# Kernel tuning notes

Hardware: AMD Instinct MI355X
Metric: run time of the kernel (lower is better)

The kernel has to match this reference:

```python
import jax, jax.numpy as jnp
import numpy as np

TAU = 0.07
COS_EPS = 1e-8   # torch F.cosine_similarity eps
L1_EPS = 1e-12   # torch F.normalize eps
MM_EPS = 1e-8    # min-max renorm eps

B, C, H, W = 64, 256, 32, 32
S, D = 512, 256


def setup_inputs() -> dict:
    key = jax.random.key(0)
    k1, k2, k3, k4 = jax.random.split(key, 4)
    scale = 1.0 / np.sqrt(D)
    return {
        "image_patches": jax.random.normal(k1, (B, C, H, W), dtype=jnp.float32),
        "text_tokens": jax.random.normal(k2, (B, S, D), dtype=jnp.float32),
        "Wv": jax.random.normal(k3, (D, D), dtype=jnp.float32) * scale,
        "bv": jnp.zeros((D,), dtype=jnp.float32),
        "Wt": jax.random.normal(k4, (D, D), dtype=jnp.float32) * scale,
        "bt": jnp.zeros((D,), dtype=jnp.float32),
    }


def _linear(x, Wgt, b):
    return x @ Wgt.T + b


def _l2n(x, axis=-1):
    n = jnp.maximum(jnp.linalg.norm(x, axis=axis, keepdims=True), COS_EPS)
    return x / n


def _sym_ce_diag(sim):
    # sim [..., N, N]; mean of -log_softmax diagonals along both class axes
    lsm_r = jax.nn.log_softmax(sim, axis=-1)
    lsm_c = jax.nn.log_softmax(sim, axis=-2)
    d_r = jnp.diagonal(lsm_r, axis1=-2, axis2=-1)
    d_c = jnp.diagonal(lsm_c, axis1=-2, axis2=-1)
    return 0.5 * (-jnp.mean(d_r) - jnp.mean(d_c))


def reference(image_patches, text_tokens, Wv, bv, Wt, bt):
    b, c, h, w = image_patches.shape
    hw = h * w
    # b c h w -> b (h w) c, then adapters
    patches = image_patches.reshape(b, c, hw).transpose(0, 2, 1)  # [b, hw, c]
    patches = _linear(patches, Wv, bv)          # [b, hw, d]
    tokens = _linear(text_tokens, Wt, bt)       # [b, s, d]

    # global embeddings: mean-pool then adapter (adapter applied twice on vision path)
    g_img = _linear(jnp.mean(patches, axis=1), Wv, bv)  # [b, d]
    g_txt = _linear(jnp.mean(tokens, axis=1), Wt, bt)   # [b, d]

    # global contrastive loss (cosine sim / tau, symmetric CE over batch)
    g_sim = (_l2n(g_img) @ _l2n(g_txt).T) / TAU         # [b, b]
    global_loss = _sym_ce_diag(g_sim)

    # fine-grained alignment
    sim = jnp.einsum('bpd,bsd->bps', patches, tokens)   # [b, hw, s]
    mn = jnp.min(sim, axis=1, keepdims=True)
    mx = jnp.max(sim, axis=1, keepdims=True)
    sim = (sim - mn) / (mx - mn + MM_EPS)
    sigma = 1.0 / hw
    sim = jnp.where(sim < sigma, 0.0, sim)
    # L1 normalize over patch dim (torch F.normalize p=1 dim=1)
    weights = sim / jnp.maximum(jnp.sum(jnp.abs(sim), axis=1, keepdims=True), L1_EPS)
    lgve = jnp.einsum('bps,bpd->bsd', weights, patches)  # [b, s, d]

    # fine-grained contrastive loss: cosine sim between grouped-vision and text tokens
    f_sim = jnp.einsum('bid,bjd->bij', _l2n(lgve), _l2n(tokens)) / TAU  # [b, s, s]
    fine_loss = _sym_ce_diag(f_sim)

    return global_loss + fine_loss
```

## Files before the change

kernel.cpp:

```cpp
#include <hip/hip_runtime.h>
#include <math.h>

#define BB   64
#define HWP  1024
#define SS   512
#define DD   256
#define TAU_INV (1.0f/0.07f)
#define SIGMA   (1.0f/1024.0f)

typedef unsigned short us;
typedef __attribute__((ext_vector_type(8))) short short8v;
typedef __attribute__((ext_vector_type(8))) unsigned short ushort8v;
typedef __attribute__((ext_vector_type(4))) float floatx4;

__device__ __forceinline__ float bf2f(us u) {
    return __uint_as_float((unsigned)u << 16);
}
__device__ __forceinline__ us f2bf(float f) {
    unsigned u = __float_as_uint(f);
    u += 0x7FFFu + ((u >> 16) & 1u);
    return (us)(u >> 16);
}
__device__ __forceinline__ void split_bf(float v, us& h, us& l) {
    h = f2bf(v);
    l = f2bf(v - bf2f(h));
}

__global__ void zero_out_k(float* out) { if (threadIdx.x == 0) out[0] = 0.0f; }

enum { OPM_F32_ROW = 0, OPM_F32_COL = 1, OPM_SPL_ROW = 2, OPM_SPL_COL = 3,
       OPM_B16_COL = 4, OPM_B16_ROW = 5, OPM_WGT_COL = 6 };
enum { OUT_F32 = 0, OUT_B16 = 1 };

#define LDSTRIDE 40

template<int MODE, int ROWS>
__device__ __forceinline__ void stage_tile(
    const char* p0, const char* p1, int ld, int row0, int k0,
    us* ldsH, us* ldsL, int tid,
    const float* wlo, const float* whi)
{
    #pragma unroll
    for (int rr = 0; rr < ROWS / 128; ++rr) {
        if constexpr (MODE == OPM_SPL_ROW) {
            const us* ph = (const us*)p0;
            const us* pl = (const us*)p1;
            const int i = rr * 128 + (tid >> 1), ko = (tid & 1) * 16;
            const long long g = (long long)(row0 + i) * ld + k0 + ko;
            *(ushort8v*)&ldsH[i * LDSTRIDE + ko]     = *(const ushort8v*)&ph[g];
            *(ushort8v*)&ldsH[i * LDSTRIDE + ko + 8] = *(const ushort8v*)&ph[g + 8];
            *(ushort8v*)&ldsL[i * LDSTRIDE + ko]     = *(const ushort8v*)&pl[g];
            *(ushort8v*)&ldsL[i * LDSTRIDE + ko + 8] = *(const ushort8v*)&pl[g + 8];
        } else if constexpr (MODE == OPM_B16_ROW) {
            const us* ph = (const us*)p0;
            const int i = rr * 128 + (tid >> 1), ko = (tid & 1) * 16;
            const long long g = (long long)(row0 + i) * ld + k0 + ko;
            *(ushort8v*)&ldsH[i * LDSTRIDE + ko]     = *(const ushort8v*)&ph[g];
            *(ushort8v*)&ldsH[i * LDSTRIDE + ko + 8] = *(const ushort8v*)&ph[g + 8];
        } else if constexpr (MODE == OPM_F32_ROW) {
            const float* pf = (const float*)p0;
            const int i = rr * 128 + (tid >> 1), ko = (tid & 1) * 16;
            const long long g = (long long)(row0 + i) * ld + k0 + ko;
            us h16[16], l16a[16];
            #pragma unroll
            for (int c = 0; c < 16; c += 4) {
                float4 v = *(const float4*)&pf[g + c];
                split_bf(v.x, h16[c+0], l16a[c+0]); split_bf(v.y, h16[c+1], l16a[c+1]);
                split_bf(v.z, h16[c+2], l16a[c+2]); split_bf(v.w, h16[c+3], l16a[c+3]);
            }
            *(ushort8v*)&ldsH[i * LDSTRIDE + ko]     = *(const ushort8v*)&h16[0];
            *(ushort8v*)&ldsH[i * LDSTRIDE + ko + 8] = *(const ushort8v*)&h16[8];
            *(ushort8v*)&ldsL[i * LDSTRIDE + ko]     = *(const ushort8v*)&l16a[0];
            *(ushort8v*)&ldsL[i * LDSTRIDE + ko + 8] = *(const ushort8v*)&l16a[8];
        } else if constexpr (MODE == OPM_F32_COL) {
            const float* pf = (const float*)p0;
            const int m = rr * 128 + (tid & 127), kh = (tid >> 7) * 16;
            const long long base = (long long)(k0 + kh) * ld + row0 + m;
            us vh[16], vl[16];
            #pragma unroll
            for (int kk = 0; kk < 16; ++kk)
                split_bf(pf[base + (long long)kk * ld], vh[kk], vl[kk]);
            *(ushort8v*)&ldsH[m * LDSTRIDE + kh]     = *(const ushort8v*)&vh[0];
            *(ushort8v*)&ldsH[m * LDSTRIDE + kh + 8] = *(const ushort8v*)&vh[8];
            *(ushort8v*)&ldsL[m * LDSTRIDE + kh]     = *(const ushort8v*)&vl[0];
            *(ushort8v*)&ldsL[m * LDSTRIDE + kh + 8] = *(const ushort8v*)&vl[8];
        } else if constexpr (MODE == OPM_B16_COL) {
            const us* ph = (const us*)p0;
            const int m = rr * 128 + (tid & 127), kh = (tid >> 7) * 16;
            const long long base = (long long)(k0 + kh) * ld + row0 + m;
            us v[16];
            #pragma unroll
            for (int kk = 0; kk < 16; ++kk)
                v[kk] = ph[base + (long long)kk * ld];
            *(ushort8v*)&ldsH[m * LDSTRIDE + kh]     = *(const ushort8v*)&v[0];
            *(ushort8v*)&ldsH[m * LDSTRIDE + kh + 8] = *(const ushort8v*)&v[8];
        } else if constexpr (MODE == OPM_WGT_COL) {
            const us* ph = (const us*)p0;
            const int m = rr * 128 + (tid & 127), kh = (tid >> 7) * 16;
            const float lo = wlo[row0 + m];
            const float inv = 1.0f / (whi[row0 + m] - lo + 1e-8f);
            const long long base = (long long)(k0 + kh) * ld + row0 + m;
            us v[16];
            #pragma unroll
            for (int kk = 0; kk < 16; ++kk) {
                const float w = (bf2f(ph[base + (long long)kk * ld]) - lo) * inv;
                v[kk] = (w < SIGMA) ? (us)0 : f2bf(w);
            }
            *(ushort8v*)&ldsH[m * LDSTRIDE + kh]     = *(const ushort8v*)&v[0];
            *(ushort8v*)&ldsH[m * LDSTRIDE + kh + 8] = *(const ushort8v*)&v[8];
        }
    }
}

template<int AMODE, int BMODE, int OMODE, int EPI, int NT>
__global__ __launch_bounds__(256) void mfma_gemm(
    const void* A0, const void* A1, const void* B0, const void* B1, void* C0,
    int M, int N, int K, int lda, int ldb, int ldc,
    long long sA, long long sB, long long sC,
    const float* __restrict__ bias, const float* __restrict__ invm,
    const float* __restrict__ invn, float scale,
    const float* __restrict__ wlo, const float* __restrict__ whi,
    float* __restrict__ aux0, float* __restrict__ aux1,
    float* __restrict__ aux2, float* __restrict__ aux3, float* __restrict__ aux4)
{
    constexpr bool ASPL = (AMODE <= OPM_SPL_COL);
    constexpr bool BSPL = (BMODE <= OPM_SPL_COL);
    constexpr int NF = NT / 16;
    __shared__ __align__(16) us Ah[128 * LDSTRIDE];
    __shared__ __align__(16) us Al[ASPL ? 128 * LDSTRIDE : 8];
    __shared__ __align__(16) us Bh[NT * LDSTRIDE];
    __shared__ __align__(16) us Bl[BSPL ? NT * LDSTRIDE : 8];
    __shared__ float redm[(EPI >= 3) ? 4 * NT : 1];
    __shared__ float reds[(EPI >= 3) ? 4 * NT : 1];

    const int tid = threadIdx.x;
    const int w = tid >> 6, lane = tid & 63;
    const int quad = lane >> 4, l16 = lane & 15;
    const int m0 = blockIdx.x * 128, n0 = blockIdx.y * NT;
    const int b = blockIdx.z;

    const char* Ab0 = (const char*)A0 + (long long)b * sA;
    const char* Ab1 = A1 ? (const char*)A1 + (long long)b * sA : nullptr;
    const char* Bb0 = (const char*)B0 + (long long)b * sB;
    const char* Bb1 = B1 ? (const char*)B1 + (long long)b * sB : nullptr;
    const float* wloA = wlo ? wlo + (long long)b * M : nullptr;
    const float* whiA = whi ? whi + (long long)b * M : nullptr;

    floatx4 acc[2][NF];
    #pragma unroll
    for (int mi = 0; mi < 2; ++mi)
        #pragma unroll
        for (int ni = 0; ni < NF; ++ni)
            acc[mi][ni] = (floatx4){0.f, 0.f, 0.f, 0.f};

    for (int k0 = 0; k0 < K; k0 += 32) {
        stage_tile<AMODE, 128>(Ab0, Ab1, lda, m0, k0, Ah, Al, tid, wloA, whiA);
        stage_tile<BMODE, NT>(Bb0, Bb1, ldb, n0, k0, Bh, Bl, tid, nullptr, nullptr);
        __syncthreads();

        short8v ah[2], al[2];
        #pragma unroll
        for (int mi = 0; mi < 2; ++mi) {
            const int r = (32 * w + 16 * mi + l16) * LDSTRIDE + quad * 8;
            ah[mi] = *(const short8v*)&Ah[r];
            if constexpr (ASPL) al[mi] = *(const short8v*)&Al[r];
        }
        #pragma unroll
        for (int ni = 0; ni < NF; ++ni) {
            const int rB = (16 * ni + l16) * LDSTRIDE + quad * 8;
            short8v bh = *(const short8v*)&Bh[rB];
            acc[0][ni] = __builtin_amdgcn_mfma_f32_16x16x32_bf16(ah[0], bh, acc[0][ni], 0, 0, 0);
            acc[1][ni] = __builtin_amdgcn_mfma_f32_16x16x32_bf16(ah[1], bh, acc[1][ni], 0, 0, 0);
            if constexpr (BSPL) {
                short8v bl = *(const short8v*)&Bl[rB];
                acc[0][ni] = __builtin_amdgcn_mfma_f32_16x16x32_bf16(ah[0], bl, acc[0][ni], 0, 0, 0);
                acc[1][ni] = __builtin_amdgcn_mfma_f32_16x16x32_bf16(ah[1], bl, acc[1][ni], 0, 0, 0);
            }
            if constexpr (ASPL) {
                acc[0][ni] = __builtin_amdgcn_mfma_f32_16x16x32_bf16(al[0], bh, acc[0][ni], 0, 0, 0);
                acc[1][ni] = __builtin_amdgcn_mfma_f32_16x16x32_bf16(al[1], bh, acc[1][ni], 0, 0, 0);
            }
        }
        __syncthreads();
    }

    if constexpr (EPI != 4) {
        char* Cb0 = (char*)C0 + (long long)b * sC;
        #pragma unroll
        for (int mi = 0; mi < 2; ++mi)
            #pragma unroll
            for (int ni = 0; ni < NF; ++ni)
                #pragma unroll
                for (int r = 0; r < 4; ++r) {
                    const int row = m0 + 32 * w + 16 * mi + quad * 4 + r;
                    const int col = n0 + 16 * ni + l16;
                    float v = acc[mi][ni][r];
                    if constexpr (EPI == 1) v += bias[col];
                    const long long idx = (long long)row * ldc + col;
                    if constexpr (OMODE == OUT_F32) ((float*)Cb0)[idx] = v;
                    else                            ((us*)Cb0)[idx] = f2bf(v);
                }
    }

    if constexpr (EPI == 3) {
        #pragma unroll
        for (int ni = 0; ni < NF; ++ni) {
            float lo = 1e30f, hi = -1e30f;
            #pragma unroll
            for (int mi = 0; mi < 2; ++mi)
                #pragma unroll
                for (int r = 0; r < 4; ++r) {
                    const float vr = bf2f(f2bf(acc[mi][ni][r]));
                    lo = fminf(lo, vr); hi = fmaxf(hi, vr);
                }
            lo = fminf(lo, __shfl_xor(lo, 16)); lo = fminf(lo, __shfl_xor(lo, 32));
            hi = fmaxf(hi, __shfl_xor(hi, 16)); hi = fmaxf(hi, __shfl_xor(hi, 32));
            if (quad == 0) {
                redm[w * NT + 16 * ni + l16] = lo;
                reds[w * NT + 16 * ni + l16] = hi;
            }
        }
        __syncthreads();
        if (tid < NT) {
            float lo = 1e30f, hi = -1e30f;
            #pragma unroll
            for (int w4 = 0; w4 < 4; ++w4) {
                lo = fminf(lo, redm[w4 * NT + tid]);
                hi = fmaxf(hi, reds[w4 * NT + tid]);
            }
            const long long o = ((long long)b * N + n0 + tid) * 8 + blockIdx.x;
            aux0[o] = lo; aux1[o] = hi;
        }
    }

    if constexpr (EPI == 4) {
        float bn[NF];
        #pragma unroll
        for (int ni = 0; ni < NF; ++ni)
            bn[ni] = invn[(long long)b * N + n0 + 16 * ni + l16] * scale;
        float amv[8];
        #pragma unroll
        for (int mi = 0; mi < 2; ++mi)
            #pragma unroll
            for (int r = 0; r < 4; ++r)
                amv[mi * 4 + r] = invm[(long long)b * M + m0 + 32 * w + 16 * mi + quad * 4 + r];

        #pragma unroll
        for (int mi = 0; mi < 2; ++mi)
            #pragma unroll
            for (int r = 0; r < 4; ++r) {
                const int grow = m0 + 32 * w + 16 * mi + quad * 4 + r;
                float vv[NF];
                float rm = -1e30f;
                #pragma unroll
                for (int ni = 0; ni < NF; ++ni) {
                    const float v = acc[mi][ni][r] * amv[mi * 4 + r] * bn[ni];
                    vv[ni] = v;
                    rm = fmaxf(rm, v);
                    if (grow == n0 + 16 * ni + l16)
                        aux4[(long long)b * M + grow] = v;
                }
                #pragma unroll
                for (int o = 8; o > 0; o >>= 1) rm = fmaxf(rm, __shfl_xor(rm, o));
                float rs = 0.f;
                #pragma unroll
                for (int ni = 0; ni < NF; ++ni) rs += expf(vv[ni] - rm);
                #pragma unroll
                for (int o = 8; o > 0; o >>= 1) rs += __shfl_xor(rs, o);
                if (l16 == 0) {
                    const long long o = ((long long)b * M + grow) * 4 + blockIdx.y;
                    aux0[o] = rm; aux1[o] = rs;
                }
            }

        #pragma unroll
        for (int ni = 0; ni < NF; ++ni) {
            float va[8];
            float cm = -1e30f;
            #pragma unroll
            for (int mi = 0; mi < 2; ++mi)
                #pragma unroll
                for (int r = 0; r < 4; ++r) {
                    const float v = acc[mi][ni][r] * amv[mi * 4 + r] * bn[ni];
                    va[mi * 4 + r] = v;
                    cm = fmaxf(cm, v);
                }
            cm = fmaxf(cm, __shfl_xor(cm, 16));
            cm = fmaxf(cm, __shfl_xor(cm, 32));
            float cs = 0.f;
            #pragma unroll
            for (int j = 0; j < 8; ++j) cs += expf(va[j] - cm);
            cs += __shfl_xor(cs, 16);
            cs += __shfl_xor(cs, 32);
            if (quad == 0) {
                redm[w * NT + 16 * ni + l16] = cm;
                reds[w * NT + 16 * ni + l16] = cs;
            }
        }
        __syncthreads();
        if (tid < NT) {
            float m = -1e30f, s = 0.f;
            #pragma unroll
            for (int w4 = 0; w4 < 4; ++w4) {
                const float cm = redm[w4 * NT + tid], cs = reds[w4 * NT + tid];
                const float nm = fmaxf(m, cm);
                s = s * expf(m - nm) + cs * expf(cm - nm);
                m = nm;
            }
            const long long o = ((long long)b * N + n0 + tid) * 4 + blockIdx.x;
            aux2[o] = m; aux3[o] = s;
        }
    }
}


__global__ __launch_bounds__(256) void convert_w_k(
    const float* Wv, const float* Wt, us* Wvh, us* Wvl, us* Wth, us* Wtl)
{
    const int i = blockIdx.x * 256 + threadIdx.x;
    split_bf(Wv[i], Wvh[i], Wvl[i]);
    split_bf(Wt[i], Wth[i], Wtl[i]);
}

__global__ __launch_bounds__(256) void mean_img_k(
    const float* __restrict__ img, float* __restrict__ mimg)
{
    const int row = blockIdx.x * 4 + (threadIdx.x >> 6);
    const int lane = threadIdx.x & 63;
    const float* p = img + (long long)row * 1024;
    float s = 0.f;
    #pragma unroll
    for (int c = 0; c < 4; ++c) {
        float4 v = *(const float4*)&p[(c * 64 + lane) * 4];
        s += v.x + v.y + v.z + v.w;
    }
    #pragma unroll
    for (int o = 32; o > 0; o >>= 1) s += __shfl_xor(s, o);
    if (lane == 0) mimg[row] = s * (1.0f / 1024.0f);
}

__global__ __launch_bounds__(256) void mean_text_s1(
    const float* __restrict__ text, float* __restrict__ part)
{
    const int b = blockIdx.x, ch = blockIdx.y, k = threadIdx.x;
    const float* p = text + ((long long)b * 512 + ch * 64) * 256 + k;
    float s = 0.f;
    for (int r = 0; r < 64; ++r) s += p[r * 256];
    part[(b * 8 + ch) * 256 + k] = s;
}
__global__ __launch_bounds__(256) void mean_text_s2(
    const float* __restrict__ part, float* __restrict__ mt)
{
    const int b = blockIdx.x, k = threadIdx.x;
    float s = 0.f;
    for (int c = 0; c < 8; ++c) s += part[(b * 8 + c) * 256 + k];
    mt[b * 256 + k] = s * (1.0f / 512.0f);
}

__global__ __launch_bounds__(256) void small_adapter_k(
    const float* __restrict__ x, const float* __restrict__ W,
    const float* __restrict__ bias, float* __restrict__ y)
{
    const int b = blockIdx.x, d = threadIdx.x;
    __shared__ float xs[256];
    xs[d] = x[b * 256 + d];
    __syncthreads();
    const float* w = W + (long long)d * 256;
    float s = bias[d];
    for (int k = 0; k < 256; ++k) s += xs[k] * w[k];
    y[b * 256 + d] = s;
}


__global__ __launch_bounds__(256) void inv_norm_f32_k(
    const float* __restrict__ x, float* __restrict__ inv)
{
    const int row = blockIdx.x * 4 + (threadIdx.x >> 6);
    const int lane = threadIdx.x & 63;
    float4 v = *(const float4*)&x[(long long)row * 256 + lane * 4];
    float s = v.x * v.x + v.y * v.y + v.z * v.z + v.w * v.w;
    #pragma unroll
    for (int o = 32; o > 0; o >>= 1) s += __shfl_xor(s, o);
    if (lane == 0) inv[row] = 1.0f / fmaxf(sqrtf(s), 1e-8f);
}

__global__ __launch_bounds__(256) void g_sim_k(
    const float* __restrict__ gi, const float* __restrict__ gt,
    const float* __restrict__ invI, const float* __restrict__ invT,
    float* __restrict__ gs)
{
    const int i = blockIdx.x, t = threadIdx.x;
    const int j = t >> 2, part = t & 3;
    __shared__ float a[256];
    a[t] = gi[i * 256 + t];
    __syncthreads();
    const float* bp = gt + (long long)j * 256 + part * 64;
    const float* ap = a + part * 64;
    float s = 0.f;
    #pragma unroll 16
    for (int k = 0; k < 64; ++k) s += ap[k] * bp[k];
    s += __shfl_xor(s, 1);
    s += __shfl_xor(s, 2);
    if (part == 0) gs[i * 64 + j] = s * invI[i] * invT[j] * TAU_INV;
}

__global__ __launch_bounds__(64) void g_lse_k(
    const float* __restrict__ gs, float* __restrict__ out)
{
    const int b = blockIdx.x, lane = threadIdx.x;
    const bool is_col = b >= 64;
    const int r = is_col ? b - 64 : b;
    const float v = is_col ? gs[lane * 64 + r] : gs[r * 64 + lane];
    float m = v;
    #pragma unroll
    for (int o = 32; o > 0; o >>= 1) m = fmaxf(m, __shfl_xor(m, o));
    float s = expf(v - m);
    #pragma unroll
    for (int o = 32; o > 0; o >>= 1) s += __shfl_xor(s, o);
    if (lane == 0)
        atomicAdd(out, ((m + logf(s)) - gs[r * 64 + r]) * (0.5f / 64.0f));
}

__global__ __launch_bounds__(256) void inv_norm_b16_k(
    const us* __restrict__ x, float* __restrict__ inv)
{
    const int row = blockIdx.x * 4 + (threadIdx.x >> 6);
    const int lane = threadIdx.x & 63;
    ushort4 h = *(const ushort4*)&x[(long long)row * 256 + lane * 4];
    const float x0 = bf2f(h.x), x1 = bf2f(h.y), x2 = bf2f(h.z), x3 = bf2f(h.w);
    float s = x0 * x0 + x1 * x1 + x2 * x2 + x3 * x3;
    #pragma unroll
    for (int o = 32; o > 0; o >>= 1) s += __shfl_xor(s, o);
    if (lane == 0) inv[row] = 1.0f / fmaxf(sqrtf(s), 1e-8f);
}


__global__ __launch_bounds__(256) void minmax_merge_k(
    const float* __restrict__ mnp, const float* __restrict__ mxp,
    float* __restrict__ mn, float* __restrict__ mx)
{
    const int idx = blockIdx.x * 256 + threadIdx.x;
    float lo = 1e30f, hi = -1e30f;
    #pragma unroll
    for (int c = 0; c < 8; ++c) {
        lo = fminf(lo, mnp[(long long)idx * 8 + c]);
        hi = fmaxf(hi, mxp[(long long)idx * 8 + c]);
    }
    mn[idx] = lo; mx[idx] = hi;
}

__global__ __launch_bounds__(256) void fine_merge4_k(
    const float* __restrict__ pm, const float* __restrict__ ps,
    const float* __restrict__ diag, float* __restrict__ out)
{
    const int idx = blockIdx.x * 256 + threadIdx.x;
    float m = -1e30f, s = 0.f;
    #pragma unroll
    for (int c = 0; c < 4; ++c) {
        const float cm = pm[(long long)idx * 4 + c], cs = ps[(long long)idx * 4 + c];
        const float nm = fmaxf(m, cm);
        s = s * expf(m - nm) + cs * expf(cm - nm);
        m = nm;
    }
    const float contrib = (m + logf(s)) - diag[idx];
    __shared__ float red[256];
    red[threadIdx.x] = contrib;
    __syncthreads();
    for (int w = 128; w > 0; w >>= 1) {
        if (threadIdx.x < w) red[threadIdx.x] += red[threadIdx.x + w];
        __syncthreads();
    }
    if (threadIdx.x == 0) atomicAdd(out, red[0] * (0.5f / (64.0f * 512.0f)));
}

extern "C" void kernel_launch(void* const* d_in, const int* in_sizes, int n_in,
                              void* d_out, int out_size, void* d_ws, size_t ws_size,
                              hipStream_t stream)
{
    const float* img  = (const float*)d_in[0];
    const float* text = (const float*)d_in[1];
    const float* Wv   = (const float*)d_in[2];
    const float* bv   = (const float*)d_in[3];
    const float* Wt   = (const float*)d_in[4];
    const float* bt   = (const float*)d_in[5];
    float* out = (float*)d_out;
    char* ws = (char*)d_ws;

    us* patches = (us*)(ws + 0);
    us* tokens  = (us*)(ws + 33554432);
    us* simW    = (us*)(ws + 50331648);
    us* lgve    = (us*)(ws + 117440512);
    char* st = ws + 134217728;
    float* mean_img  = (float*)(st + 0);
    float* mean_text = (float*)(st + 65536);
    float* mean_pat  = (float*)(st + 131072);
    float* mean_tok  = (float*)(st + 196608);
    float* g_img     = (float*)(st + 262144);
    float* g_txt     = (float*)(st + 327680);
    float* textpart  = (float*)(st + 393216);
    float* mnp       = (float*)(st + 917504);
    float* mxp       = (float*)(st + 1966080);
    float* mnv       = (float*)(st + 3014656);
    float* mxv       = (float*)(st + 3145728);
    float* inv_l     = (float*)(st + 3276800);
    float* inv_t     = (float*)(st + 3407872);
    us* Wvh = (us*)(st + 3538944);
    us* Wvl = (us*)(st + 3670016);
    us* Wth = (us*)(st + 3801088);
    us* Wtl = (us*)(st + 3932160);
    float* inv_gi  = (float*)(st + 4063232);
    float* inv_gt  = (float*)(st + 4063744);
    float* g_simbf = (float*)(st + 4064256);
    float* pm_row  = (float*)(st + 4194304);
    float* ps_row  = (float*)(st + 4718592);
    float* pm_col  = (float*)(st + 5242880);
    float* ps_col  = (float*)(st + 5767168);
    float* diag    = (float*)(st + 6291456);

    zero_out_k<<<1, 64, 0, stream>>>(out);
    convert_w_k<<<256, 256, 0, stream>>>(Wv, Wt, Wvh, Wvl, Wth, Wtl);

    mean_img_k<<<4096, 256, 0, stream>>>(img, mean_img);
    mean_text_s1<<<dim3(64, 8), 256, 0, stream>>>(text, textpart);
    mean_text_s2<<<64, 256, 0, stream>>>(textpart, mean_text);
    small_adapter_k<<<BB, 256, 0, stream>>>(mean_img, Wv, bv, mean_pat);
    small_adapter_k<<<BB, 256, 0, stream>>>(mean_pat, Wv, bv, g_img);
    small_adapter_k<<<BB, 256, 0, stream>>>(mean_text, Wt, bt, mean_tok);
    small_adapter_k<<<BB, 256, 0, stream>>>(mean_tok, Wt, bt, g_txt);
    inv_norm_f32_k<<<16, 256, 0, stream>>>(g_img, inv_gi);
    inv_norm_f32_k<<<16, 256, 0, stream>>>(g_txt, inv_gt);
    g_sim_k<<<64, 256, 0, stream>>>(g_img, g_txt, inv_gi, inv_gt, g_simbf);
    g_lse_k<<<128, 64, 0, stream>>>(g_simbf, out);

    mfma_gemm<OPM_F32_COL, OPM_SPL_ROW, OUT_B16, 1, 256><<<dim3(8, 1, BB), 256, 0, stream>>>(
        img, nullptr, Wvh, Wvl, patches,
        1024, 256, 256, 1024, 256, 256,
        1048576LL, 0LL, 524288LL, bv, nullptr, nullptr, 0.f, nullptr, nullptr,
        nullptr, nullptr, nullptr, nullptr, nullptr);

    mfma_gemm<OPM_F32_ROW, OPM_SPL_ROW, OUT_B16, 1, 256><<<dim3(4, 1, BB), 256, 0, stream>>>(
        text, nullptr, Wth, Wtl, tokens,
        512, 256, 256, 256, 256, 256,
        524288LL, 0LL, 262144LL, bt, nullptr, nullptr, 0.f, nullptr, nullptr,
        nullptr, nullptr, nullptr, nullptr, nullptr);

    mfma_gemm<OPM_B16_ROW, OPM_B16_ROW, OUT_B16, 3, 128><<<dim3(8, 4, BB), 256, 0, stream>>>(
        patches, nullptr, tokens, nullptr, simW,
        1024, 512, 256, 256, 256, 512,
        524288LL, 262144LL, 1048576LL, nullptr, nullptr, nullptr, 0.f, nullptr, nullptr,
        mnp, mxp, nullptr, nullptr, nullptr);

    minmax_merge_k<<<128, 256, 0, stream>>>(mnp, mxp, mnv, mxv);

    mfma_gemm<OPM_WGT_COL, OPM_B16_COL, OUT_B16, 0, 128><<<dim3(4, 2, BB), 256, 0, stream>>>(
        simW, nullptr, patches, nullptr, lgve,
        512, 256, 1024, 512, 256, 256,
        1048576LL, 524288LL, 262144LL, nullptr, nullptr, nullptr, 0.f, mnv, mxv,
        nullptr, nullptr, nullptr, nullptr, nullptr);

    inv_norm_b16_k<<<8192, 256, 0, stream>>>(lgve, inv_l);
    inv_norm_b16_k<<<8192, 256, 0, stream>>>(tokens, inv_t);

    mfma_gemm<OPM_B16_ROW, OPM_B16_ROW, OUT_B16, 4, 128><<<dim3(4, 4, BB), 256, 0, stream>>>(
        lgve, nullptr, tokens, nullptr, nullptr,
        512, 512, 256, 256, 256, 512,
        262144LL, 262144LL, 0LL, nullptr, inv_l, inv_t, TAU_INV, nullptr, nullptr,
        pm_row, ps_row, pm_col, ps_col, diag);

    fine_merge4_k<<<128, 256, 0, stream>>>(pm_row, ps_row, diag, out);
    fine_merge4_k<<<128, 256, 0, stream>>>(pm_col, ps_col, diag, out);
}
```

Baseline: 416.9 us.

## Prefetch next K-tile into registers and remap workgroups across XCDs in GEMM

Splits tile staging into a global-to-register load and a register-to-LDS store, so that for three GEMMs the next K tile's global loads are issued before the MFMA work on the current tile. Workgroup IDs are remapped so consecutive logical tiles land on the same XCD for better L2 locality. The per-row min/max normalisation values are now loaded once per block instead of once per K step, and the small adapter dot product is vectorised with float4. The prefetch raises register pressure, which may lower occupancy.

```diff
diff --git a/kernel.cpp b/kernel.cpp
--- a/kernel.cpp
+++ b/kernel.cpp
@@ -35,10 +35,18 @@
 #define LDSTRIDE 40
 
 template<int MODE, int ROWS>
-__device__ __forceinline__ void stage_tile(
-    const char* p0, const char* p1, int ld, int row0, int k0,
-    us* ldsH, us* ldsL, int tid,
-    const float* wlo, const float* whi)
+struct SRegs {
+    static constexpr int RR = ROWS / 128;
+    static constexpr bool ISF32 = (MODE == OPM_F32_ROW) || (MODE == OPM_F32_COL);
+    ushort8v h[ISF32 ? 1 : RR][2];
+    ushort8v l[(MODE == OPM_SPL_ROW) ? RR : 1][2];
+    float4   f[ISF32 ? RR : 1][4];
+};
+
+template<int MODE, int ROWS>
+__device__ __forceinline__ void stage_load(
+    const char* p0, const char* p1, int ld, int row0, int k0, int tid,
+    SRegs<MODE, ROWS>& R)
 {
     #pragma unroll
     for (int rr = 0; rr < ROWS / 128; ++rr) {
@@ -47,72 +55,116 @@
             const us* pl = (const us*)p1;
             const int i = rr * 128 + (tid >> 1), ko = (tid & 1) * 16;
             const long long g = (long long)(row0 + i) * ld + k0 + ko;
-            *(ushort8v*)&ldsH[i * LDSTRIDE + ko]     = *(const ushort8v*)&ph[g];
-            *(ushort8v*)&ldsH[i * LDSTRIDE + ko + 8] = *(const ushort8v*)&ph[g + 8];
-            *(ushort8v*)&ldsL[i * LDSTRIDE + ko]     = *(const ushort8v*)&pl[g];
-            *(ushort8v*)&ldsL[i * LDSTRIDE + ko + 8] = *(const ushort8v*)&pl[g + 8];
+            R.h[rr][0] = *(const ushort8v*)&ph[g];
+            R.h[rr][1] = *(const ushort8v*)&ph[g + 8];
+            R.l[rr][0] = *(const ushort8v*)&pl[g];
+            R.l[rr][1] = *(const ushort8v*)&pl[g + 8];
         } else if constexpr (MODE == OPM_B16_ROW) {
             const us* ph = (const us*)p0;
             const int i = rr * 128 + (tid >> 1), ko = (tid & 1) * 16;
             const long long g = (long long)(row0 + i) * ld + k0 + ko;
-            *(ushort8v*)&ldsH[i * LDSTRIDE + ko]     = *(const ushort8v*)&ph[g];
-            *(ushort8v*)&ldsH[i * LDSTRIDE + ko + 8] = *(const ushort8v*)&ph[g + 8];
+            R.h[rr][0] = *(const ushort8v*)&ph[g];
+            R.h[rr][1] = *(const ushort8v*)&ph[g + 8];
         } else if constexpr (MODE == OPM_F32_ROW) {
             const float* pf = (const float*)p0;
             const int i = rr * 128 + (tid >> 1), ko = (tid & 1) * 16;
             const long long g = (long long)(row0 + i) * ld + k0 + ko;
+            #pragma unroll
+            for (int c = 0; c < 4; ++c)
+                R.f[rr][c] = *(const float4*)&pf[g + c * 4];
+        } else if constexpr (MODE == OPM_F32_COL) {
+            const float* pf = (const float*)p0;
+            const int m = rr * 128 + (tid & 127), kh = (tid >> 7) * 16;
+            const long long base = (long long)(k0 + kh) * ld + row0 + m;
+            #pragma unroll
+            for (int c = 0; c < 4; ++c) {
+                float4 v;
+                v.x = pf[base + (long long)(c * 4 + 0) * ld];
+                v.y = pf[base + (long long)(c * 4 + 1) * ld];
+                v.z = pf[base + (long long)(c * 4 + 2) * ld];
+                v.w = pf[base + (long long)(c * 4 + 3) * ld];
+                R.f[rr][c] = v;
+            }
+        } else {
+            const us* ph = (const us*)p0;
+            const int m = rr * 128 + (tid & 127), kh = (tid >> 7) * 16;
+            const long long base = (long long)(k0 + kh) * ld + row0 + m;
+            #pragma unroll
+            for (int kk = 0; kk < 8; ++kk) {
+                R.h[rr][0][kk] = ph[base + (long long)kk * ld];
+                R.h[rr][1][kk] = ph[base + (long long)(kk + 8) * ld];
+            }
+        }
+    }
+}
+
+template<int MODE, int ROWS>
+__device__ __forceinline__ void stage_store(
+    const SRegs<MODE, ROWS>& R, us* ldsH, us* ldsL, int tid, float lo, float inv)
+{
+    #pragma unroll
+    for (int rr = 0; rr < ROWS / 128; ++rr) {
+        if constexpr (MODE == OPM_SPL_ROW) {
+            const int i = rr * 128 + (tid >> 1), ko = (tid & 1) * 16;
+            *(ushort8v*)&ldsH[i * LDSTRIDE + ko]     = R.h[rr][0];
+            *(ushort8v*)&ldsH[i * LDSTRIDE + ko + 8] = R.h[rr][1];
+            *(ushort8v*)&ldsL[i * LDSTRIDE + ko]     = R.l[rr][0];
+            *(ushort8v*)&ldsL[i * LDSTRIDE + ko + 8] = R.l[rr][1];
+        } else if constexpr (MODE == OPM_B16_ROW) {
+            const int i = rr * 128 + (tid >> 1), ko = (tid & 1) * 16;
+            *(ushort8v*)&ldsH[i * LDSTRIDE + ko]     = R.h[rr][0];
+            *(ushort8v*)&ldsH[i * LDSTRIDE + ko + 8] = R.h[rr][1];
+        } else if constexpr (MODE == OPM_F32_ROW) {
+            const int i = rr * 128 + (tid >> 1), ko = (tid & 1) * 16;
             us h16[16], l16a[16];
             #pragma unroll
-            for (int c = 0; c < 16; c += 4) {
-                float4 v = *(const float4*)&pf[g + c];
-                split_bf(v.x, h16[c+0], l16a[c+0]); split_bf(v.y, h16[c+1], l16a[c+1]);
-                split_bf(v.z, h16[c+2], l16a[c+2]); split_bf(v.w, h16[c+3], l16a[c+3]);
+            for (int c = 0; c < 4; ++c) {
+                float4 v = R.f[rr][c];
+                split_bf(v.x, h16[c*4+0], l16a[c*4+0]);
+                split_bf(v.y, h16[c*4+1], l16a[c*4+1]);
+                split_bf(v.z, h16[c*4+2], l16a[c*4+2]);
+                split_bf(v.w, h16[c*4+3], l16a[c*4+3]);
             }
             *(ushort8v*)&ldsH[i * LDSTRIDE + ko]     = *(const ushort8v*)&h16[0];
             *(ushort8v*)&ldsH[i * LDSTRIDE + ko + 8] = *(const ushort8v*)&h16[8];
             *(ushort8v*)&ldsL[i * LDSTRIDE + ko]     = *(const ushort8v*)&l16a[0];
             *(ushort8v*)&ldsL[i * LDSTRIDE + ko + 8] = *(const ushort8v*)&l16a[8];
         } else if constexpr (MODE == OPM_F32_COL) {
-            const float* pf = (const float*)p0;
             const int m = rr * 128 + (tid & 127), kh = (tid >> 7) * 16;
-            const long long base = (long long)(k0 + kh) * ld + row0 + m;
             us vh[16], vl[16];
             #pragma unroll
-            for (int kk = 0; kk < 16; ++kk)
-                split_bf(pf[base + (long long)kk * ld], vh[kk], vl[kk]);
+            for (int c = 0; c < 4; ++c) {
+                float4 v = R.f[rr][c];
+                split_bf(v.x, vh[c*4+0], vl[c*4+0]);
+                split_bf(v.y, vh[c*4+1], vl[c*4+1]);
+                split_bf(v.z, vh[c*4+2], vl[c*4+2]);
+                split_bf(v.w, vh[c*4+3], vl[c*4+3]);
+            }
             *(ushort8v*)&ldsH[m * LDSTRIDE + kh]     = *(const ushort8v*)&vh[0];
             *(ushort8v*)&ldsH[m * LDSTRIDE + kh + 8] = *(const ushort8v*)&vh[8];
             *(ushort8v*)&ldsL[m * LDSTRIDE + kh]     = *(const ushort8v*)&vl[0];
             *(ushort8v*)&ldsL[m * LDSTRIDE + kh + 8] = *(const ushort8v*)&vl[8];
         } else if constexpr (MODE == OPM_B16_COL) {
-            const us* ph = (const us*)p0;
             const int m = rr * 128 + (tid & 127), kh = (tid >> 7) * 16;
-            const long long base = (long long)(k0 + kh) * ld + row0 + m;
+            *(ushort8v*)&ldsH[m * LDSTRIDE + kh]     = R.h[rr][0];
+            *(ushort8v*)&ldsH[m * LDSTRIDE + kh + 8] = R.h[rr][1];
+        } else if constexpr (MODE == OPM_WGT_COL) {
+            const int m = rr * 128 + (tid & 127), kh = (tid >> 7) * 16;
             us v[16];
             #pragma unroll
-            for (int kk = 0; kk < 16; ++kk)
-                v[kk] = ph[base + (long long)kk * ld];
+            for (int kk = 0; kk < 8; ++kk) {
+                const float w0 = (bf2f(R.h[rr][0][kk]) - lo) * inv;
+                const float w1 = (bf2f(R.h[rr][1][kk]) - lo) * inv;
+                v[kk]     = (w0 < SIGMA) ? (us)0 : f2bf(w0);
+                v[kk + 8] = (w1 < SIGMA) ? (us)0 : f2bf(w1);
+            }
             *(ushort8v*)&ldsH[m * LDSTRIDE + kh]     = *(const ushort8v*)&v[0];
             *(ushort8v*)&ldsH[m * LDSTRIDE + kh + 8] = *(const ushort8v*)&v[8];
-        } else if constexpr (MODE == OPM_WGT_COL) {
-            const us* ph = (const us*)p0;
-            const int m = rr * 128 + (tid & 127), kh = (tid >> 7) * 16;
-            const float lo = wlo[row0 + m];
-            const float inv = 1.0f / (whi[row0 + m] - lo + 1e-8f);
-            const long long base = (long long)(k0 + kh) * ld + row0 + m;
-            us v[16];
-            #pragma unroll
-            for (int kk = 0; kk < 16; ++kk) {
-                const float w = (bf2f(ph[base + (long long)kk * ld]) - lo) * inv;
-                v[kk] = (w < SIGMA) ? (us)0 : f2bf(w);
-            }
-            *(ushort8v*)&ldsH[m * LDSTRIDE + kh]     = *(const ushort8v*)&v[0];
-            *(ushort8v*)&ldsH[m * LDSTRIDE + kh + 8] = *(const ushort8v*)&v[8];
-        }
-    }
-}
-
-template<int AMODE, int BMODE, int OMODE, int EPI, int NT>
+        }
+    }
+}
+
+template<int AMODE, int BMODE, int OMODE, int EPI, int NT, int PREF>
 __global__ __launch_bounds__(256) void mfma_gemm(
     const void* A0, const void* A1, const void* B0, const void* B1, void* C0,
     int M, int N, int K, int lda, int ldb, int ldc,
@@ -136,15 +188,42 @@
     const int tid = threadIdx.x;
     const int w = tid >> 6, lane = tid & 63;
     const int quad = lane >> 4, l16 = lane & 15;
-    const int m0 = blockIdx.x * 128, n0 = blockIdx.y * NT;
-    const int b = blockIdx.z;
+
+    int bx = blockIdx.x, by = blockIdx.y, bz = blockIdx.z;
+    {
+        const int nbx = gridDim.x, nby = gridDim.y, nbz = gridDim.z;
+        const int nwg = nbx * nby * nbz;
+        if ((nwg & 7) == 0) {
+            const int hw = bx + nbx * (by + nby * bz);
+            const int cpx = nwg >> 3;
+            int wk = (hw & 7) * cpx + (hw >> 3);
+            bx = wk % nbx; wk /= nbx;
+            by = wk % nby; bz = wk / nby;
+        }
+    }
+
+    const int m0 = bx * 128, n0 = by * NT;
+    const int b = bz;
 
     const char* Ab0 = (const char*)A0 + (long long)b * sA;
     const char* Ab1 = A1 ? (const char*)A1 + (long long)b * sA : nullptr;
     const char* Bb0 = (const char*)B0 + (long long)b * sB;
     const char* Bb1 = B1 ? (const char*)B1 + (long long)b * sB : nullptr;
-    const float* wloA = wlo ? wlo + (long long)b * M : nullptr;
-    const float* whiA = whi ? whi + (long long)b * M : nullptr;
+
+    float loA = 0.f, invA = 0.f;
+    if constexpr (AMODE == OPM_WGT_COL) {
+        const float* wloA = wlo + (long long)b * M;
+        const float* whiA = whi + (long long)b * M;
+        loA = wloA[m0 + (tid & 127)];
+        invA = 1.0f / (whiA[m0 + (tid & 127)] - loA + 1e-8f);
+    }
+
+    SRegs<AMODE, 128> RA;
+    SRegs<BMODE, NT>  RB;
+    if constexpr (PREF) {
+        stage_load<AMODE, 128>(Ab0, Ab1, lda, m0, 0, tid, RA);
+        stage_load<BMODE, NT>(Bb0, Bb1, ldb, n0, 0, tid, RB);
+    }
 
     floatx4 acc[2][NF];
     #pragma unroll
@@ -154,9 +233,20 @@
             acc[mi][ni] = (floatx4){0.f, 0.f, 0.f, 0.f};
 
     for (int k0 = 0; k0 < K; k0 += 32) {
-        stage_tile<AMODE, 128>(Ab0, Ab1, lda, m0, k0, Ah, Al, tid, wloA, whiA);
-        stage_tile<BMODE, NT>(Bb0, Bb1, ldb, n0, k0, Bh, Bl, tid, nullptr, nullptr);
+        if constexpr (!PREF) {
+            stage_load<AMODE, 128>(Ab0, Ab1, lda, m0, k0, tid, RA);
+            stage_load<BMODE, NT>(Bb0, Bb1, ldb, n0, k0, tid, RB);
+        }
+        stage_store<AMODE, 128>(RA, Ah, Al, tid, loA, invA);
+        stage_store<BMODE, NT>(RB, Bh, Bl, tid, 0.f, 0.f);
         __syncthreads();
+
+        if constexpr (PREF) {
+            if (k0 + 32 < K) {
+                stage_load<AMODE, 128>(Ab0, Ab1, lda, m0, k0 + 32, tid, RA);
+                stage_load<BMODE, NT>(Bb0, Bb1, ldb, n0, k0 + 32, tid, RB);
+            }
+        }
 
         short8v ah[2], al[2];
         #pragma unroll
@@ -228,7 +318,7 @@
                 lo = fminf(lo, redm[w4 * NT + tid]);
                 hi = fmaxf(hi, reds[w4 * NT + tid]);
             }
-            const long long o = ((long long)b * N + n0 + tid) * 8 + blockIdx.x;
+            const long long o = ((long long)b * N + n0 + tid) * 8 + bx;
             aux0[o] = lo; aux1[o] = hi;
         }
     }
@@ -268,7 +358,7 @@
                 #pragma unroll
                 for (int o = 8; o > 0; o >>= 1) rs += __shfl_xor(rs, o);
                 if (l16 == 0) {
-                    const long long o = ((long long)b * M + grow) * 4 + blockIdx.y;
+                    const long long o = ((long long)b * M + grow) * 4 + by;
                     aux0[o] = rm; aux1[o] = rs;
                 }
             }
@@ -307,7 +397,7 @@
                 s = s * expf(m - nm) + cs * expf(cm - nm);
                 m = nm;
             }
-            const long long o = ((long long)b * N + n0 + tid) * 4 + blockIdx.x;
+            const long long o = ((long long)b * N + n0 + tid) * 4 + bx;
             aux2[o] = m; aux3[o] = s;
         }
     }
@@ -365,9 +455,14 @@
     __shared__ float xs[256];
     xs[d] = x[b * 256 + d];
     __syncthreads();
-    const float* w = W + (long long)d * 256;
+    const float4* w = (const float4*)(W + (long long)d * 256);
+    const float4* xv = (const float4*)xs;
     float s = bias[d];
-    for (int k = 0; k < 256; ++k) s += xs[k] * w[k];
+    #pragma unroll 8
+    for (int k = 0; k < 64; ++k) {
+        const float4 a = xv[k], ww = w[k];
+        s += a.x * ww.x + a.y * ww.y + a.z * ww.z + a.w * ww.w;
+    }
     y[b * 256 + d] = s;
 }
 
@@ -532,19 +627,19 @@
     g_sim_k<<<64, 256, 0, stream>>>(g_img, g_txt, inv_gi, inv_gt, g_simbf);
     g_lse_k<<<128, 64, 0, stream>>>(g_simbf, out);
 
-    mfma_gemm<OPM_F32_COL, OPM_SPL_ROW, OUT_B16, 1, 256><<<dim3(8, 1, BB), 256, 0, stream>>>(
+    mfma_gemm<OPM_F32_COL, OPM_SPL_ROW, OUT_B16, 1, 256, 0><<<dim3(8, 1, BB), 256, 0, stream>>>(
         img, nullptr, Wvh, Wvl, patches,
         1024, 256, 256, 1024, 256, 256,
         1048576LL, 0LL, 524288LL, bv, nullptr, nullptr, 0.f, nullptr, nullptr,
         nullptr, nullptr, nullptr, nullptr, nullptr);
 
-    mfma_gemm<OPM_F32_ROW, OPM_SPL_ROW, OUT_B16, 1, 256><<<dim3(4, 1, BB), 256, 0, stream>>>(
+    mfma_gemm<OPM_F32_ROW, OPM_SPL_ROW, OUT_B16, 1, 256, 0><<<dim3(4, 1, BB), 256, 0, stream>>>(
         text, nullptr, Wth, Wtl, tokens,
         512, 256, 256, 256, 256, 256,
         524288LL, 0LL, 262144LL, bt, nullptr, nullptr, 0.f, nullptr, nullptr,
         nullptr, nullptr, nullptr, nullptr, nullptr);
 
-    mfma_gemm<OPM_B16_ROW, OPM_B16_ROW, OUT_B16, 3, 128><<<dim3(8, 4, BB), 256, 0, stream>>>(
+    mfma_gemm<OPM_B16_ROW, OPM_B16_ROW, OUT_B16, 3, 128, 1><<<dim3(8, 4, BB), 256, 0, stream>>>(
         patches, nullptr, tokens, nullptr, simW,
         1024, 512, 256, 256, 256, 512,
         524288LL, 262144LL, 1048576LL, nullptr, nullptr, nullptr, 0.f, nullptr, nullptr,
@@ -552,7 +647,7 @@
 
     minmax_merge_k<<<128, 256, 0, stream>>>(mnp, mxp, mnv, mxv);
 
-    mfma_gemm<OPM_WGT_COL, OPM_B16_COL, OUT_B16, 0, 128><<<dim3(4, 2, BB), 256, 0, stream>>>(
+    mfma_gemm<OPM_WGT_COL, OPM_B16_COL, OUT_B16, 0, 128, 1><<<dim3(4, 2, BB), 256, 0, stream>>>(
         simW, nullptr, patches, nullptr, lgve,
         512, 256, 1024, 512, 256, 256,
         1048576LL, 524288LL, 262144LL, nullptr, nullptr, nullptr, 0.f, mnv, mxv,
@@ -561,7 +656,7 @@
     inv_norm_b16_k<<<8192, 256, 0, stream>>>(lgve, inv_l);
     inv_norm_b16_k<<<8192, 256, 0, stream>>>(tokens, inv_t);
 
-    mfma_gemm<OPM_B16_ROW, OPM_B16_ROW, OUT_B16, 4, 128><<<dim3(4, 4, BB), 256, 0, stream>>>(
+    mfma_gemm<OPM_B16_ROW, OPM_B16_ROW, OUT_B16, 4, 128, 1><<<dim3(4, 4, BB), 256, 0, stream>>>(
         lgve, nullptr, tokens, nullptr, nullptr,
         512, 512, 256, 256, 256, 512,
         262144LL, 262144LL, 0LL, nullptr, inv_l, inv_t, TAU_INV, nullptr, nullptr,
```

Result: faster. 402.8 us (-3.4%).
